# Kernel optimization log

Hardware: AMD Instinct MI355X
Metric: run time of the kernel (lower is better)

Reference implementation:

```python
import math
import jax, jax.numpy as jnp
import numpy as np

L = 2          # num_layers
B = 2          # micro batch
S = 2048       # seq_length
H = 1024       # hidden_size
NH = 16        # num_attention_heads
DH = 64        # kv_channels (head dim)
FF = 4096      # ffn_hidden_size
EPS = 1e-5
STD = 0.0048


def setup_inputs() -> dict:
    key = jax.random.key(0)
    ks = jax.random.split(key, 12)
    out_std = STD / math.sqrt(2.0 * L)
    # ALiBi slopes for NH=16 (power of 2)
    start = 2.0 ** (-2.0 ** (-(math.log2(NH) - 3)))
    slopes = np.array([start * start ** i for i in range(NH)], dtype=np.float32)
    alibi = slopes[None, :, None, None] * np.arange(S, dtype=np.float32)[None, None, None, :]
    alibi = jnp.asarray(np.broadcast_to(alibi, (B, NH, 1, S)))  # [B, NH, 1, S]
    return {
        "hidden_states": jax.random.normal(ks[0], (B, S, H), jnp.float32),
        "alibi": alibi,
        "qkv_w": jax.random.normal(ks[1], (L, 3 * NH * DH, H), jnp.float32) * STD,
        "qkv_b": jnp.zeros((L, 3 * NH * DH), jnp.float32),
        "dense_w": jax.random.normal(ks[2], (L, H, NH * DH), jnp.float32) * out_std,
        "dense_b": jnp.zeros((L, H), jnp.float32),
        "mlp_w1": jax.random.normal(ks[3], (L, FF, H), jnp.float32) * STD,
        "mlp_b1": jnp.zeros((L, FF), jnp.float32),
        "mlp_w2": jax.random.normal(ks[4], (L, H, FF), jnp.float32) * out_std,
        "mlp_b2": jnp.zeros((L, H), jnp.float32),
        "ln1_w": jnp.ones((L, H), jnp.float32),
        "ln1_b": jnp.zeros((L, H), jnp.float32),
        "ln2_w": jnp.ones((L, H), jnp.float32),
        "ln2_b": jnp.zeros((L, H), jnp.float32),
    }


def _layernorm(x, w, b):
    mu = jnp.mean(x, axis=-1, keepdims=True)
    var = jnp.mean(jnp.square(x - mu), axis=-1, keepdims=True)
    return (x - mu) * jax.lax.rsqrt(var + EPS) * w + b


def _layer(x, alibi, causal, layer_number, qkv_w, qkv_b, dense_w, dense_b,
           mlp_w1, mlp_b1, mlp_w2, mlp_b2, ln1_w, ln1_b, ln2_w, ln2_b):
    # --- attention ---
    h = _layernorm(x, ln1_w, ln1_b)
    qkv = h @ qkv_w.T + qkv_b                       # [B, S, 3*NH*DH]
    q, k, v = jnp.split(qkv, 3, axis=-1)
    q = q.reshape(B, S, NH, DH).transpose(0, 2, 1, 3)  # [B, NH, S, DH]
    k = k.reshape(B, S, NH, DH).transpose(0, 2, 1, 3)
    v = v.reshape(B, S, NH, DH).transpose(0, 2, 1, 3)
    norm_factor = math.sqrt(DH) * layer_number
    beta = 1.0 / layer_number
    alpha = 1.0 / norm_factor
    scores = beta * alibi + alpha * jnp.einsum("bhqd,bhkd->bhqk", q, k)
    # ScaleMaskSoftmax: scale by layer_number, causal mask fill -10000, softmax
    scores = scores * layer_number
    scores = jnp.where(causal, scores, jnp.float32(-10000.0))
    probs = jax.nn.softmax(scores, axis=-1)
    ctx = jnp.einsum("bhqk,bhkd->bhqd", probs, v)   # [B, NH, S, DH]
    ctx = ctx.transpose(0, 2, 1, 3).reshape(B, S, NH * DH)
    attn_out = ctx @ dense_w.T + dense_b
    x = x + attn_out
    # --- MLP ---
    h2 = _layernorm(x, ln2_w, ln2_b)
    m = jax.nn.gelu(h2 @ mlp_w1.T + mlp_b1, approximate=False)
    m = m @ mlp_w2.T + mlp_b2
    return x + m


def reference(hidden_states, alibi, qkv_w, qkv_b, dense_w, dense_b,
              mlp_w1, mlp_b1, mlp_w2, mlp_b2, ln1_w, ln1_b, ln2_w, ln2_b):
    causal = jnp.tril(jnp.ones((S, S), dtype=bool))[None, None]  # [1,1,S,S]
    x = hidden_states
    for l in range(L):
        x = _layer(x, alibi, causal, l + 1,
                   qkv_w[l], qkv_b[l], dense_w[l], dense_b[l],
                   mlp_w1[l], mlp_b1[l], mlp_w2[l], mlp_b2[l],
                   ln1_w[l], ln1_b[l], ln2_w[l], ln2_b[l])
    return x
```

## Files before the change

kernel.cpp:

```cpp
#include <hip/hip_runtime.h>
#include <cstdint>
#include <cmath>

#define SS 2048
#define HH 1024

typedef __bf16 bf16_t;
typedef __bf16 bf16x8 __attribute__((ext_vector_type(8)));
typedef __bf16 bf16x4 __attribute__((ext_vector_type(4)));
typedef float  f32x4  __attribute__((ext_vector_type(4)));

union U32P { unsigned u; bf16_t h[2]; };

__device__ __forceinline__ void async_load16(const void* g, void* l) {
  __builtin_amdgcn_global_load_lds(
      (__attribute__((address_space(1))) void*)(g),
      (__attribute__((address_space(3))) void*)(l), 16, 0, 0);
}

__global__ __launch_bounds__(256) void cvt_kernel(const float* __restrict__ in,
                                                  bf16_t* __restrict__ out) {
  size_t i = (size_t)blockIdx.x * 256 + threadIdx.x;
  f32x4 v = ((const f32x4*)in)[i];
  bf16x4 o;
  o[0] = (bf16_t)v[0]; o[1] = (bf16_t)v[1]; o[2] = (bf16_t)v[2]; o[3] = (bf16_t)v[3];
  ((bf16x4*)out)[i] = o;
}

__global__ __launch_bounds__(256) void ln_kernel(const float* __restrict__ x,
                                                 const float* __restrict__ w,
                                                 const float* __restrict__ b,
                                                 bf16_t* __restrict__ out) {
  const int row = blockIdx.x;
  const int tid = threadIdx.x;
  const f32x4 v = ((const f32x4*)(x + (size_t)row * HH))[tid];
  float s  = v[0] + v[1] + v[2] + v[3];
  float s2 = v[0]*v[0] + v[1]*v[1] + v[2]*v[2] + v[3]*v[3];
#pragma unroll
  for (int o = 1; o < 64; o <<= 1) { s += __shfl_xor(s, o); s2 += __shfl_xor(s2, o); }
  __shared__ float r1[4], r2[4];
  if ((tid & 63) == 0) { r1[tid >> 6] = s; r2[tid >> 6] = s2; }
  __syncthreads();
  float ts  = r1[0] + r1[1] + r1[2] + r1[3];
  float ts2 = r2[0] + r2[1] + r2[2] + r2[3];
  float mu  = ts * (1.0f / HH);
  float var = ts2 * (1.0f / HH) - mu * mu;
  float rstd = rsqrtf(var + 1e-5f);
  f32x4 wv = ((const f32x4*)w)[tid];
  f32x4 bv = ((const f32x4*)b)[tid];
  bf16x4 o;
#pragma unroll
  for (int j = 0; j < 4; ++j) o[j] = (bf16_t)((v[j] - mu) * rstd * wv[j] + bv[j]);
  ((bf16x4*)(out + (size_t)row * HH))[tid] = o;
}

__device__ __forceinline__ float gelu_f(float x) {
  return 0.5f * x * (1.0f + erff(x * 0.70710678118654752f));
}

template <int EPI>
__global__ __launch_bounds__(256) void gemm_bt(const bf16_t* __restrict__ A,
                                               const bf16_t* __restrict__ W,
                                               const float* __restrict__ bias,
                                               const float* __restrict__ res,
                                               bf16_t* __restrict__ outb,
                                               float* __restrict__ outf,
                                               int M, int N, int K) {
  __shared__ __align__(16) bf16_t As[128 * 64];
  __shared__ __align__(16) bf16_t Bs[128 * 64];
  const int tid = threadIdx.x;
  const int w = tid >> 6, lane = tid & 63;
  const int m16 = lane & 15, quad = lane >> 4;
  const int wm = w & 1, wn = w >> 1;
  const int n0 = blockIdx.x * 128, m0 = blockIdx.y * 128;

  f32x4 acc[4][4];
#pragma unroll
  for (int i = 0; i < 4; ++i)
#pragma unroll
    for (int j = 0; j < 4; ++j) acc[i][j] = (f32x4){0.f, 0.f, 0.f, 0.f};

  int rowi[4], gci[4];
#pragma unroll
  for (int i = 0; i < 4; ++i) {
    int p = (w * 4 + i) * 64 + lane;
    rowi[i] = p >> 3;
    gci[i] = ((lane & 7) ^ (rowi[i] & 7)) * 8;
  }

  for (int kt = 0; kt < K; kt += 64) {
    __syncthreads();
#pragma unroll
    for (int i = 0; i < 4; ++i) {
      async_load16(A + (size_t)(m0 + rowi[i]) * K + kt + gci[i], &As[(w * 4 + i) * 512]);
      async_load16(W + (size_t)(n0 + rowi[i]) * K + kt + gci[i], &Bs[(w * 4 + i) * 512]);
    }
    __syncthreads();
#pragma unroll
    for (int kk = 0; kk < 2; ++kk) {
      bf16x8 af[4], bfv[4];
#pragma unroll
      for (int mi = 0; mi < 4; ++mi) {
        int row = wm * 64 + mi * 16 + m16;
        int cpos = (kk * 4 + quad) ^ (row & 7);
        af[mi] = *(const bf16x8*)&As[row * 64 + cpos * 8];
      }
#pragma unroll
      for (int ni = 0; ni < 4; ++ni) {
        int row = wn * 64 + ni * 16 + m16;
        int cpos = (kk * 4 + quad) ^ (row & 7);
        bfv[ni] = *(const bf16x8*)&Bs[row * 64 + cpos * 8];
      }
#pragma unroll
      for (int mi = 0; mi < 4; ++mi)
#pragma unroll
        for (int ni = 0; ni < 4; ++ni)
          acc[mi][ni] = __builtin_amdgcn_mfma_f32_16x16x32_bf16(af[mi], bfv[ni],
                                                                acc[mi][ni], 0, 0, 0);
    }
  }

#pragma unroll
  for (int ni = 0; ni < 4; ++ni) {
    int col = n0 + wn * 64 + ni * 16 + m16;
    float bv = bias[col];
#pragma unroll
    for (int mi = 0; mi < 4; ++mi) {
      int rowb = m0 + wm * 64 + mi * 16 + quad * 4;
#pragma unroll
      for (int r = 0; r < 4; ++r) {
        size_t idx = (size_t)(rowb + r) * N + col;
        float v = acc[mi][ni][r] + bv;
        if constexpr (EPI == 1) v = gelu_f(v);
        if constexpr (EPI == 2) outf[idx] = v + res[idx];
        else outb[idx] = (bf16_t)v;
      }
    }
  }
}

__global__ __launch_bounds__(256) void attn_kernel(const bf16_t* __restrict__ qkv,
                                                   bf16_t* __restrict__ ctx) {
  const int qt = 31 - blockIdx.y;
  const int bh = blockIdx.x;
  const int b = bh >> 4, h = bh & 15;
  const int tid = threadIdx.x;
  const int w = tid >> 6, lane = tid & 63;
  const int m16 = lane & 15, quad = lane >> 4;

  __shared__ __align__(16) bf16_t Vt[64 * 72];
  __shared__ __align__(16) bf16_t Pl[4][16 * 72];

  const float slope2 = __builtin_amdgcn_exp2f(-0.70710678118654752f * (float)(h + 1))
                       * 1.4426950408889634f;
  float alk[16];
#pragma unroll
  for (int kn = 0; kn < 4; ++kn)
#pragma unroll
    for (int r = 0; r < 4; ++r)
      alk[kn * 4 + r] = slope2 * (float)(kn * 16 + quad * 4 + r);

  const int qrow = qt * 64 + w * 16 + m16;
  const bf16_t* qbase = qkv + (size_t)(b * SS + qrow) * 3072 + h * 64;
  const bf16x8 bq0 = *(const bf16x8*)(qbase + quad * 8);
  const bf16x8 bq1 = *(const bf16x8*)(qbase + 32 + quad * 8);

  const bf16_t* kbase = qkv + (size_t)(b * SS + m16) * 3072 + 1024 + h * 64 + quad * 8;

  f32x4 acc[4];
#pragma unroll
  for (int i = 0; i < 4; ++i) acc[i] = (f32x4){0.f, 0.f, 0.f, 0.f};
  float m_run = -INFINITY, l_run = 0.f;

  const int kp2 = (tid & 31) * 2, vd0 = (tid >> 5) * 8;
  const bf16_t* vsrc = qkv + (size_t)(b * SS + kp2) * 3072 + 2048 + h * 64 + vd0;
  const int ql = w * 16 + m16;
  constexpr float C = 0.18033688011112042f;

  bf16x8 v0 = *(const bf16x8*)(vsrc);
  bf16x8 v1 = *(const bf16x8*)(vsrc + 3072);

  for (int kt = 0; kt <= qt; ++kt) {
    __syncthreads();
#pragma unroll
    for (int j = 0; j < 8; ++j) {
      U32P pk; pk.h[0] = v0[j]; pk.h[1] = v1[j];
      *(unsigned*)&Vt[(vd0 + j) * 72 + kp2] = pk.u;
    }
    __syncthreads();
    bf16x8 nv0 = v0, nv1 = v1;
    if (kt < qt) {
      const bf16_t* nsrc = vsrc + (size_t)(kt + 1) * 64 * 3072;
      nv0 = *(const bf16x8*)(nsrc);
      nv1 = *(const bf16x8*)(nsrc + 3072);
    }

    const bf16_t* kb = kbase + (size_t)kt * 64 * 3072;
    float s2[16];
    float mx = -INFINITY;
    const bool diag = (kt == qt);
#pragma unroll
    for (int kn = 0; kn < 4; ++kn) {
      bf16x8 ak0 = *(const bf16x8*)(kb + (size_t)(kn * 16) * 3072);
      bf16x8 ak1 = *(const bf16x8*)(kb + (size_t)(kn * 16) * 3072 + 32);
      f32x4 z = (f32x4){0.f, 0.f, 0.f, 0.f};
      z = __builtin_amdgcn_mfma_f32_16x16x32_bf16(ak0, bq0, z, 0, 0, 0);
      z = __builtin_amdgcn_mfma_f32_16x16x32_bf16(ak1, bq1, z, 0, 0, 0);
#pragma unroll
      for (int r = 0; r < 4; ++r) {
        float s = fmaf(z[r], C, alk[kn * 4 + r]);
        if (diag) {
          int kl = kn * 16 + quad * 4 + r;
          if (kl > ql) s = -INFINITY;
        }
        s2[kn * 4 + r] = s;
        mx = fmaxf(mx, s);
      }
    }
    mx = fmaxf(mx, __shfl_xor(mx, 16));
    mx = fmaxf(mx, __shfl_xor(mx, 32));
    const float base_t = slope2 * (float)(kt * 64);
    const float m_abs = mx + base_t;
    const float m_new = fmaxf(m_run, m_abs);
    const float alpha = __builtin_amdgcn_exp2f(m_run - m_new);
    const float msub = m_new - base_t;
    float rs = 0.f;
    float p[16];
#pragma unroll
    for (int i = 0; i < 16; ++i) {
      p[i] = __builtin_amdgcn_exp2f(s2[i] - msub);
      rs += p[i];
    }
    rs += __shfl_xor(rs, 16);
    rs += __shfl_xor(rs, 32);
    l_run = l_run * alpha + rs;
    m_run = m_new;
#pragma unroll
    for (int ni = 0; ni < 4; ++ni) acc[ni] *= alpha;

#pragma unroll
    for (int kn = 0; kn < 4; ++kn) {
      U32P a, c;
      a.h[0] = (bf16_t)p[kn * 4 + 0]; a.h[1] = (bf16_t)p[kn * 4 + 1];
      c.h[0] = (bf16_t)p[kn * 4 + 2]; c.h[1] = (bf16_t)p[kn * 4 + 3];
      uint2 pk; pk.x = a.u; pk.y = c.u;
      *(uint2*)&Pl[w][m16 * 72 + kn * 16 + quad * 4] = pk;
    }
    bf16x8 bp0 = *(const bf16x8*)&Pl[w][m16 * 72 + quad * 8];
    bf16x8 bp1 = *(const bf16x8*)&Pl[w][m16 * 72 + 32 + quad * 8];
#pragma unroll
    for (int ni = 0; ni < 4; ++ni) {
      bf16x8 av0 = *(const bf16x8*)&Vt[(ni * 16 + m16) * 72 + quad * 8];
      bf16x8 av1 = *(const bf16x8*)&Vt[(ni * 16 + m16) * 72 + 32 + quad * 8];
      acc[ni] = __builtin_amdgcn_mfma_f32_16x16x32_bf16(av0, bp0, acc[ni], 0, 0, 0);
      acc[ni] = __builtin_amdgcn_mfma_f32_16x16x32_bf16(av1, bp1, acc[ni], 0, 0, 0);
    }
    v0 = nv0; v1 = nv1;
  }

  const float inv_l = 1.0f / l_run;
  bf16_t* cb = ctx + (size_t)(b * SS + qt * 64 + w * 16 + m16) * 1024 + h * 64;
#pragma unroll
  for (int ni = 0; ni < 4; ++ni) {
    U32P a, c;
    a.h[0] = (bf16_t)(acc[ni][0] * inv_l); a.h[1] = (bf16_t)(acc[ni][1] * inv_l);
    c.h[0] = (bf16_t)(acc[ni][2] * inv_l); c.h[1] = (bf16_t)(acc[ni][3] * inv_l);
    uint2 pk; pk.x = a.u; pk.y = c.u;
    *(uint2*)(cb + ni * 16 + quad * 4) = pk;
  }
}

extern "C" void kernel_launch(void* const* d_in, const int* in_sizes, int n_in,
                              void* d_out, int out_size, void* d_ws, size_t ws_size,
                              hipStream_t stream) {
  const float* hs    = (const float*)d_in[0];
  const float* qkvw  = (const float*)d_in[2];
  const float* qkvb  = (const float*)d_in[3];
  const float* dw    = (const float*)d_in[4];
  const float* db    = (const float*)d_in[5];
  const float* w1    = (const float*)d_in[6];
  const float* b1    = (const float*)d_in[7];
  const float* w2    = (const float*)d_in[8];
  const float* b2    = (const float*)d_in[9];
  const float* ln1w  = (const float*)d_in[10];
  const float* ln1b  = (const float*)d_in[11];
  const float* ln2w  = (const float*)d_in[12];
  const float* ln2b  = (const float*)d_in[13];
  float* x = (float*)d_out;

  char* ws = (char*)d_ws;
  bf16_t* wqc = (bf16_t*)(ws + 0);
  bf16_t* wdc = (bf16_t*)(ws + 12582912);
  bf16_t* w1c = (bf16_t*)(ws + 16777216);
  bf16_t* w2c = (bf16_t*)(ws + 33554432);
  bf16_t* hb  = (bf16_t*)(ws + 50331648);
  bf16_t* qm  = (bf16_t*)(ws + 58720256);
  bf16_t* cx  = (bf16_t*)(ws + 92274688);

  hipMemcpyAsync(x, hs, (size_t)4096 * 1024 * 4, hipMemcpyDeviceToDevice, stream);
  cvt_kernel<<<6144, 256, 0, stream>>>(qkvw, wqc);
  cvt_kernel<<<2048, 256, 0, stream>>>(dw, wdc);
  cvt_kernel<<<8192, 256, 0, stream>>>(w1, w1c);
  cvt_kernel<<<8192, 256, 0, stream>>>(w2, w2c);

  for (int l = 0; l < 2; ++l) {
    ln_kernel<<<4096, 256, 0, stream>>>(x, ln1w + l * 1024, ln1b + l * 1024, hb);
    gemm_bt<0><<<dim3(24, 32), 256, 0, stream>>>(hb, wqc + (size_t)l * 3145728,
        qkvb + l * 3072, nullptr, qm, nullptr, 4096, 3072, 1024);
    attn_kernel<<<dim3(32, 32), 256, 0, stream>>>(qm, cx);
    gemm_bt<2><<<dim3(8, 32), 256, 0, stream>>>(cx, wdc + (size_t)l * 1048576,
        db + l * 1024, x, nullptr, x, 4096, 1024, 1024);
    ln_kernel<<<4096, 256, 0, stream>>>(x, ln2w + l * 1024, ln2b + l * 1024, hb);
    gemm_bt<1><<<dim3(32, 32), 256, 0, stream>>>(hb, w1c + (size_t)l * 4194304,
        b1 + l * 4096, nullptr, qm, nullptr, 4096, 4096, 1024);
    gemm_bt<2><<<dim3(8, 32), 256, 0, stream>>>(qm, w2c + (size_t)l * 4194304,
        b2 + l * 1024, x, nullptr, x, 4096, 1024, 4096);
  }
}
```

Before: 764.2 us.

## Split-K with atomic residual accumulation for N=1024 GEMMs and double-buffer attention K/V

Replaces the residual-add GEMM epilogue with a split-K kernel that atomically adds partial products (plus bias on the first split) directly into the fp32 residual stream. This raises the block count for the narrow N=1024 GEMMs, which previously launched only 256 blocks, and so improves CU occupancy. The attention kernel now prefetches the next K tile into registers and double-buffers V in LDS, which removes one barrier per iteration, and it adds a launch bound. Atomics add memory traffic and make the summation order nondeterministic.

Measured after the change: 796.5 us. +4.2%, slower.

```diff
diff --git a/kernel.cpp b/kernel.cpp
--- a/kernel.cpp
+++ b/kernel.cpp
@@ -62,9 +62,7 @@
 __global__ __launch_bounds__(256) void gemm_bt(const bf16_t* __restrict__ A,
                                                const bf16_t* __restrict__ W,
                                                const float* __restrict__ bias,
-                                               const float* __restrict__ res,
                                                bf16_t* __restrict__ outb,
-                                               float* __restrict__ outf,
                                                int M, int N, int K) {
   __shared__ __align__(16) bf16_t As[128 * 64];
   __shared__ __align__(16) bf16_t Bs[128 * 64];
@@ -132,15 +130,91 @@
         size_t idx = (size_t)(rowb + r) * N + col;
         float v = acc[mi][ni][r] + bv;
         if constexpr (EPI == 1) v = gelu_f(v);
-        if constexpr (EPI == 2) outf[idx] = v + res[idx];
-        else outb[idx] = (bf16_t)v;
-      }
-    }
-  }
-}
-
-__global__ __launch_bounds__(256) void attn_kernel(const bf16_t* __restrict__ qkv,
-                                                   bf16_t* __restrict__ ctx) {
+        outb[idx] = (bf16_t)v;
+      }
+    }
+  }
+}
+
+__global__ __launch_bounds__(256) void gemm_bt_sk(const bf16_t* __restrict__ A,
+                                                  const bf16_t* __restrict__ W,
+                                                  const float* __restrict__ bias,
+                                                  float* __restrict__ outf,
+                                                  int M, int N, int K, int KS) {
+  __shared__ __align__(16) bf16_t As[128 * 64];
+  __shared__ __align__(16) bf16_t Bs[128 * 64];
+  const int tid = threadIdx.x;
+  const int w = tid >> 6, lane = tid & 63;
+  const int m16 = lane & 15, quad = lane >> 4;
+  const int wm = w & 1, wn = w >> 1;
+  const int n0 = blockIdx.x * 128, m0 = blockIdx.y * 128;
+  const int z = blockIdx.z;
+  const int kbeg = z * KS, kend = kbeg + KS;
+
+  f32x4 acc[4][4];
+#pragma unroll
+  for (int i = 0; i < 4; ++i)
+#pragma unroll
+    for (int j = 0; j < 4; ++j) acc[i][j] = (f32x4){0.f, 0.f, 0.f, 0.f};
+
+  int rowi[4], gci[4];
+#pragma unroll
+  for (int i = 0; i < 4; ++i) {
+    int p = (w * 4 + i) * 64 + lane;
+    rowi[i] = p >> 3;
+    gci[i] = ((lane & 7) ^ (rowi[i] & 7)) * 8;
+  }
+
+  for (int kt = kbeg; kt < kend; kt += 64) {
+    __syncthreads();
+#pragma unroll
+    for (int i = 0; i < 4; ++i) {
+      async_load16(A + (size_t)(m0 + rowi[i]) * K + kt + gci[i], &As[(w * 4 + i) * 512]);
+      async_load16(W + (size_t)(n0 + rowi[i]) * K + kt + gci[i], &Bs[(w * 4 + i) * 512]);
+    }
+    __syncthreads();
+#pragma unroll
+    for (int kk = 0; kk < 2; ++kk) {
+      bf16x8 af[4], bfv[4];
+#pragma unroll
+      for (int mi = 0; mi < 4; ++mi) {
+        int row = wm * 64 + mi * 16 + m16;
+        int cpos = (kk * 4 + quad) ^ (row & 7);
+        af[mi] = *(const bf16x8*)&As[row * 64 + cpos * 8];
+      }
+#pragma unroll
+      for (int ni = 0; ni < 4; ++ni) {
+        int row = wn * 64 + ni * 16 + m16;
+        int cpos = (kk * 4 + quad) ^ (row & 7);
+        bfv[ni] = *(const bf16x8*)&Bs[row * 64 + cpos * 8];
+      }
+#pragma unroll
+      for (int mi = 0; mi < 4; ++mi)
+#pragma unroll
+        for (int ni = 0; ni < 4; ++ni)
+          acc[mi][ni] = __builtin_amdgcn_mfma_f32_16x16x32_bf16(af[mi], bfv[ni],
+                                                                acc[mi][ni], 0, 0, 0);
+    }
+  }
+
+#pragma unroll
+  for (int ni = 0; ni < 4; ++ni) {
+    int col = n0 + wn * 64 + ni * 16 + m16;
+    float bv = (z == 0) ? bias[col] : 0.0f;
+#pragma unroll
+    for (int mi = 0; mi < 4; ++mi) {
+      int rowb = m0 + wm * 64 + mi * 16 + quad * 4;
+#pragma unroll
+      for (int r = 0; r < 4; ++r) {
+        size_t idx = (size_t)(rowb + r) * N + col;
+        atomicAdd(&outf[idx], acc[mi][ni][r] + bv);
+      }
+    }
+  }
+}
+
+__global__ __launch_bounds__(256, 2) void attn_kernel(const bf16_t* __restrict__ qkv,
+                                                      bf16_t* __restrict__ ctx) {
   const int qt = 31 - blockIdx.y;
   const int bh = blockIdx.x;
   const int b = bh >> 4, h = bh & 15;
@@ -148,7 +222,7 @@
   const int w = tid >> 6, lane = tid & 63;
   const int m16 = lane & 15, quad = lane >> 4;
 
-  __shared__ __align__(16) bf16_t Vt[64 * 72];
+  __shared__ __align__(16) bf16_t Vt[2][64 * 72];
   __shared__ __align__(16) bf16_t Pl[4][16 * 72];
 
   const float slope2 = __builtin_amdgcn_exp2f(-0.70710678118654752f * (float)(h + 1))
@@ -166,46 +240,57 @@
   const bf16x8 bq1 = *(const bf16x8*)(qbase + 32 + quad * 8);
 
   const bf16_t* kbase = qkv + (size_t)(b * SS + m16) * 3072 + 1024 + h * 64 + quad * 8;
-
-  f32x4 acc[4];
-#pragma unroll
-  for (int i = 0; i < 4; ++i) acc[i] = (f32x4){0.f, 0.f, 0.f, 0.f};
-  float m_run = -INFINITY, l_run = 0.f;
-
   const int kp2 = (tid & 31) * 2, vd0 = (tid >> 5) * 8;
   const bf16_t* vsrc = qkv + (size_t)(b * SS + kp2) * 3072 + 2048 + h * 64 + vd0;
   const int ql = w * 16 + m16;
   constexpr float C = 0.18033688011112042f;
 
-  bf16x8 v0 = *(const bf16x8*)(vsrc);
-  bf16x8 v1 = *(const bf16x8*)(vsrc + 3072);
+  f32x4 acc[4];
+#pragma unroll
+  for (int i = 0; i < 4; ++i) acc[i] = (f32x4){0.f, 0.f, 0.f, 0.f};
+  float m_run = -INFINITY, l_run = 0.f;
+
+  bf16x8 ak[4][2], v0, v1;
+#pragma unroll
+  for (int kn = 0; kn < 4; ++kn) {
+    ak[kn][0] = *(const bf16x8*)(kbase + (size_t)(kn * 16) * 3072);
+    ak[kn][1] = *(const bf16x8*)(kbase + (size_t)(kn * 16) * 3072 + 32);
+  }
+  v0 = *(const bf16x8*)(vsrc);
+  v1 = *(const bf16x8*)(vsrc + 3072);
+#pragma unroll
+  for (int j = 0; j < 8; ++j) {
+    U32P pk; pk.h[0] = v0[j]; pk.h[1] = v1[j];
+    *(unsigned*)&Vt[0][(vd0 + j) * 72 + kp2] = pk.u;
+  }
 
   for (int kt = 0; kt <= qt; ++kt) {
     __syncthreads();
-#pragma unroll
-    for (int j = 0; j < 8; ++j) {
-      U32P pk; pk.h[0] = v0[j]; pk.h[1] = v1[j];
-      *(unsigned*)&Vt[(vd0 + j) * 72 + kp2] = pk.u;
-    }
-    __syncthreads();
-    bf16x8 nv0 = v0, nv1 = v1;
+
+    bf16x8 nk[4][2], nv0 = v0, nv1 = v1;
     if (kt < qt) {
+      const bf16_t* kb = kbase + (size_t)(kt + 1) * 64 * 3072;
+#pragma unroll
+      for (int kn = 0; kn < 4; ++kn) {
+        nk[kn][0] = *(const bf16x8*)(kb + (size_t)(kn * 16) * 3072);
+        nk[kn][1] = *(const bf16x8*)(kb + (size_t)(kn * 16) * 3072 + 32);
+      }
       const bf16_t* nsrc = vsrc + (size_t)(kt + 1) * 64 * 3072;
       nv0 = *(const bf16x8*)(nsrc);
       nv1 = *(const bf16x8*)(nsrc + 3072);
-    }
-
-    const bf16_t* kb = kbase + (size_t)kt * 64 * 3072;
+    } else {
+#pragma unroll
+      for (int kn = 0; kn < 4; ++kn) { nk[kn][0] = ak[kn][0]; nk[kn][1] = ak[kn][1]; }
+    }
+
     float s2[16];
     float mx = -INFINITY;
     const bool diag = (kt == qt);
 #pragma unroll
     for (int kn = 0; kn < 4; ++kn) {
-      bf16x8 ak0 = *(const bf16x8*)(kb + (size_t)(kn * 16) * 3072);
-      bf16x8 ak1 = *(const bf16x8*)(kb + (size_t)(kn * 16) * 3072 + 32);
       f32x4 z = (f32x4){0.f, 0.f, 0.f, 0.f};
-      z = __builtin_amdgcn_mfma_f32_16x16x32_bf16(ak0, bq0, z, 0, 0, 0);
-      z = __builtin_amdgcn_mfma_f32_16x16x32_bf16(ak1, bq1, z, 0, 0, 0);
+      z = __builtin_amdgcn_mfma_f32_16x16x32_bf16(ak[kn][0], bq0, z, 0, 0, 0);
+      z = __builtin_amdgcn_mfma_f32_16x16x32_bf16(ak[kn][1], bq1, z, 0, 0, 0);
 #pragma unroll
       for (int r = 0; r < 4; ++r) {
         float s = fmaf(z[r], C, alk[kn * 4 + r]);
@@ -220,8 +305,7 @@
     mx = fmaxf(mx, __shfl_xor(mx, 16));
     mx = fmaxf(mx, __shfl_xor(mx, 32));
     const float base_t = slope2 * (float)(kt * 64);
-    const float m_abs = mx + base_t;
-    const float m_new = fmaxf(m_run, m_abs);
+    const float m_new = fmaxf(m_run, mx + base_t);
     const float alpha = __builtin_amdgcn_exp2f(m_run - m_new);
     const float msub = m_new - base_t;
     float rs = 0.f;
@@ -246,15 +330,26 @@
       uint2 pk; pk.x = a.u; pk.y = c.u;
       *(uint2*)&Pl[w][m16 * 72 + kn * 16 + quad * 4] = pk;
     }
+    const bf16_t* vt = &Vt[kt & 1][0];
     bf16x8 bp0 = *(const bf16x8*)&Pl[w][m16 * 72 + quad * 8];
     bf16x8 bp1 = *(const bf16x8*)&Pl[w][m16 * 72 + 32 + quad * 8];
 #pragma unroll
     for (int ni = 0; ni < 4; ++ni) {
-      bf16x8 av0 = *(const bf16x8*)&Vt[(ni * 16 + m16) * 72 + quad * 8];
-      bf16x8 av1 = *(const bf16x8*)&Vt[(ni * 16 + m16) * 72 + 32 + quad * 8];
+      bf16x8 av0 = *(const bf16x8*)&vt[(ni * 16 + m16) * 72 + quad * 8];
+      bf16x8 av1 = *(const bf16x8*)&vt[(ni * 16 + m16) * 72 + 32 + quad * 8];
       acc[ni] = __builtin_amdgcn_mfma_f32_16x16x32_bf16(av0, bp0, acc[ni], 0, 0, 0);
       acc[ni] = __builtin_amdgcn_mfma_f32_16x16x32_bf16(av1, bp1, acc[ni], 0, 0, 0);
     }
+
+    if (kt < qt) {
+#pragma unroll
+      for (int j = 0; j < 8; ++j) {
+        U32P pk; pk.h[0] = nv0[j]; pk.h[1] = nv1[j];
+        *(unsigned*)&Vt[(kt + 1) & 1][(vd0 + j) * 72 + kp2] = pk.u;
+      }
+    }
+#pragma unroll
+    for (int kn = 0; kn < 4; ++kn) { ak[kn][0] = nk[kn][0]; ak[kn][1] = nk[kn][1]; }
     v0 = nv0; v1 = nv1;
   }
 
@@ -306,14 +401,14 @@
   for (int l = 0; l < 2; ++l) {
     ln_kernel<<<4096, 256, 0, stream>>>(x, ln1w + l * 1024, ln1b + l * 1024, hb);
     gemm_bt<0><<<dim3(24, 32), 256, 0, stream>>>(hb, wqc + (size_t)l * 3145728,
-        qkvb + l * 3072, nullptr, qm, nullptr, 4096, 3072, 1024);
+        qkvb + l * 3072, qm, 4096, 3072, 1024);
     attn_kernel<<<dim3(32, 32), 256, 0, stream>>>(qm, cx);
-    gemm_bt<2><<<dim3(8, 32), 256, 0, stream>>>(cx, wdc + (size_t)l * 1048576,
-        db + l * 1024, x, nullptr, x, 4096, 1024, 1024);
+    gemm_bt_sk<<<dim3(8, 32, 2), 256, 0, stream>>>(cx, wdc + (size_t)l * 1048576,
+        db + l * 1024, x, 4096, 1024, 1024, 512);
     ln_kernel<<<4096, 256, 0, stream>>>(x, ln2w + l * 1024, ln2b + l * 1024, hb);
     gemm_bt<1><<<dim3(32, 32), 256, 0, stream>>>(hb, w1c + (size_t)l * 4194304,
-        b1 + l * 4096, nullptr, qm, nullptr, 4096, 4096, 1024);
-    gemm_bt<2><<<dim3(8, 32), 256, 0, stream>>>(qm, w2c + (size_t)l * 4194304,
-        b2 + l * 1024, x, nullptr, x, 4096, 1024, 4096);
-  }
-}
+        b1 + l * 4096, qm, 4096, 4096, 1024);
+    gemm_bt_sk<<<dim3(8, 32, 4), 256, 0, stream>>>(qm, w2c + (size_t)l * 4194304,
+        b2 + l * 1024, x, 4096, 1024, 4096, 1024);
+  }
+}
```
